# Optimization experiments

Hardware: AMD Instinct MI355X
Metric: run time of the kernel (lower is better)

## Reference

```python
import jax, jax.numpy as jnp
import numpy as np

N_NODES = 50000
N_EDGES = 800000
IN_DIM = 8
EDGE_DIM = 4
HIDDEN = 16
OUT_DIM = 1


def _lin_init(key, fan_in, fan_out):
    kw, kb = jax.random.split(key)
    bound = 1.0 / np.sqrt(fan_in)
    W = jax.random.uniform(kw, (fan_in, fan_out), minval=-bound, maxval=bound, dtype=jnp.float32)
    b = jax.random.uniform(kb, (fan_out,), minval=-bound, maxval=bound, dtype=jnp.float32)
    return W, b


def setup_inputs() -> dict:
    key = jax.random.key(0)
    ks = jax.random.split(key, 16)
    x = jax.random.normal(ks[0], (N_NODES, IN_DIM), dtype=jnp.float32)
    edge_index = jax.random.randint(ks[1], (2, N_EDGES), 0, N_NODES, dtype=jnp.int32)
    edge_attr = jax.random.normal(ks[2], (N_EDGES, EDGE_DIM), dtype=jnp.float32)

    inp = {"x": x, "edge_index": edge_index, "edge_attr": edge_attr}
    in_dims = [IN_DIM, HIDDEN]
    for i in range(2):
        d_in = in_dims[i]
        W1, b1 = _lin_init(ks[3 + 4 * i], EDGE_DIM, HIDDEN)
        W2, b2 = _lin_init(ks[4 + 4 * i], HIDDEN, d_in * HIDDEN)
        root = jax.random.uniform(ks[5 + 4 * i], (d_in, HIDDEN), minval=-1.0 / np.sqrt(d_in), maxval=1.0 / np.sqrt(d_in), dtype=jnp.float32)
        bias = jnp.zeros((HIDDEN,), dtype=jnp.float32)
        inp[f"eW1_{i}"] = W1; inp[f"eb1_{i}"] = b1
        inp[f"eW2_{i}"] = W2; inp[f"eb2_{i}"] = b2
        inp[f"root_{i}"] = root; inp[f"bias_{i}"] = bias
    mW1, mb1 = _lin_init(ks[11], HIDDEN, HIDDEN)
    mW2, mb2 = _lin_init(ks[12], HIDDEN, OUT_DIM)
    inp["mW1"] = mW1; inp["mb1"] = mb1; inp["mW2"] = mW2; inp["mb2"] = mb2
    return inp


def _nnconv(x, src, dst, edge_attr, eW1, eb1, eW2, eb2, root, bias):
    # edge MLP -> per-edge weight matrix [E, d_in, HIDDEN]
    h = jax.nn.silu(edge_attr @ eW1 + eb1)
    Wedge = (h @ eW2 + eb2).reshape(edge_attr.shape[0], x.shape[1], HIDDEN)
    # gather source features, per-edge matmul, scatter-mean to targets
    msg = jnp.einsum('ei,eio->eo', x[src], Wedge)  # [E, HIDDEN]
    agg = jax.ops.segment_sum(msg, dst, num_segments=N_NODES)
    cnt = jax.ops.segment_sum(jnp.ones((msg.shape[0],), dtype=msg.dtype), dst, num_segments=N_NODES)
    agg = agg / jnp.maximum(cnt, 1.0)[:, None]
    return x @ root + agg + bias


def reference(x, edge_index, edge_attr,
              eW1_0, eb1_0, eW2_0, eb2_0, root_0, bias_0,
              eW1_1, eb1_1, eW2_1, eb2_1, root_1, bias_1,
              mW1, mb1, mW2, mb2):
    src, dst = edge_index[0], edge_index[1]
    x = jax.nn.relu(_nnconv(x, src, dst, edge_attr, eW1_0, eb1_0, eW2_0, eb2_0, root_0, bias_0))
    x = jax.nn.relu(_nnconv(x, src, dst, edge_attr, eW1_1, eb1_1, eW2_1, eb2_1, root_1, bias_1))
    out = jax.nn.sigmoid(jax.nn.silu(x @ mW1 + mb1) @ mW2 + mb2)
    return out
```

## Files before the change

kernel.cpp:

```cpp
#include <hip/hip_runtime.h>
#include <hip/hip_fp16.h>

#define NN 50000
#define NE 800000
#define NBUCK 392

__device__ __forceinline__ float sigm(float v) { return 1.0f / (1.0f + __expf(-v)); }


__global__ void sort_count(const int* __restrict__ ei,
                           int* __restrict__ cntA, int* __restrict__ cntB)
{
    __shared__ int hA[NBUCK], hB[NBUCK];
    int t = threadIdx.x;
    for (int i = t; i < NBUCK; i += 256) { hA[i] = 0; hB[i] = 0; }
    __syncthreads();
    int base = blockIdx.x * 2048;
#pragma unroll
    for (int r = 0; r < 8; ++r) {
        int idx = base + r * 256 + t;
        if (idx < NE) {
            int s = ei[idx], d = ei[NE + idx];
            atomicAdd(&hB[s >> 7], 1);
            atomicAdd(&hA[d >> 7], 1);
        }
    }
    __syncthreads();
    for (int i = t; i < NBUCK; i += 256) {
        if (hA[i]) atomicAdd(&cntA[i], hA[i]);
        if (hB[i]) atomicAdd(&cntB[i], hB[i]);
    }
}

__global__ void sort_scan(const int* __restrict__ cntA, const int* __restrict__ cntB,
                          int* __restrict__ baseA, int* __restrict__ baseB,
                          int* __restrict__ curA,  int* __restrict__ curB)
{
    __shared__ int a[512], b[512];
    int t = threadIdx.x;
    a[t] = (t < NBUCK) ? cntA[t] : 0;
    b[t] = (t < NBUCK) ? cntB[t] : 0;
    __syncthreads();
#pragma unroll
    for (int dd = 1; dd < 512; dd <<= 1) {
        int av = (t >= dd) ? a[t - dd] : 0;
        int bv = (t >= dd) ? b[t - dd] : 0;
        __syncthreads();
        a[t] += av; b[t] += bv;
        __syncthreads();
    }
    int exA = (t > 0) ? a[t - 1] : 0;
    int exB = (t > 0) ? b[t - 1] : 0;
    if (t < NBUCK) { baseA[t] = exA; curA[t] = exA; baseB[t] = exB; curB[t] = exB; }
    if (t == 511)  { baseA[NBUCK] = a[511]; baseB[NBUCK] = b[511]; }
}

__global__ __launch_bounds__(256) void sort_scatterA(const int* __restrict__ ei,
                                                     int* __restrict__ curA,
                                                     unsigned long long* __restrict__ recA)
{
    __shared__ int lcnt[NBUCK];
    __shared__ int lofs[NBUCK];
    int t = threadIdx.x;
    for (int i = t; i < NBUCK; i += 256) lcnt[i] = 0;
    __syncthreads();
    int base = blockIdx.x * 2048;
#pragma unroll
    for (int r = 0; r < 8; ++r) {
        int e = base + r * 256 + t;
        if (e < NE) atomicAdd(&lcnt[ei[NE + e] >> 7], 1);
    }
    __syncthreads();
    for (int i = t; i < NBUCK; i += 256)
        lofs[i] = lcnt[i] ? atomicAdd(&curA[i], lcnt[i]) : 0;
    __syncthreads();
#pragma unroll
    for (int r = 0; r < 8; ++r) {
        int e = base + r * 256 + t;
        if (e < NE) {
            int s = ei[e], d = ei[NE + e];
            int p = atomicAdd(&lofs[d >> 7], 1);
            recA[p] = ((unsigned long long)(unsigned)(d & 127) << 36)
                    | ((unsigned long long)(unsigned)s << 20)
                    | (unsigned long long)(unsigned)e;
        }
    }
}

__global__ __launch_bounds__(256) void sort_localAB(const unsigned long long* __restrict__ recA,
                                                    const int* __restrict__ baseA,
                                                    int* __restrict__ off_all,
                                                    int* __restrict__ curB,
                                                    unsigned long long* __restrict__ recB)
{
    __shared__ int c[128];
    __shared__ int live[128];
    __shared__ int lcnt[NBUCK];
    __shared__ int lofs[NBUCK];
    int t = threadIdx.x;
    int b = blockIdx.x;
    int lo = baseA[b], hi = baseA[b + 1];
    if (t < 128) c[t] = 0;
    for (int i = t; i < NBUCK; i += 256) lcnt[i] = 0;
    __syncthreads();
    for (int i = lo + t; i < hi; i += 256) {
        unsigned long long rec = recA[i];
        atomicAdd(&c[(int)(rec >> 36) & 127], 1);
        atomicAdd(&lcnt[(int)(rec >> 27) & 511], 1);
    }
    __syncthreads();
#pragma unroll
    for (int dd = 1; dd < 128; dd <<= 1) {
        int v = (t >= dd && t < 128) ? c[t - dd] : 0;
        __syncthreads();
        if (t < 128) c[t] += v;
        __syncthreads();
    }
    if (t < 128) {
        int ex = (t > 0) ? c[t - 1] : 0;
        int d = (b << 7) + t;
        if (d <= NN) off_all[d] = lo + ex;
        live[t] = lo + ex;
    }
    __syncthreads();
    for (int i = t; i < NBUCK; i += 256)
        lofs[i] = lcnt[i] ? atomicAdd(&curB[i], lcnt[i]) : 0;
    __syncthreads();
    for (int i = lo + t; i < hi; i += 256) {
        unsigned long long rec = recA[i];
        int dp = atomicAdd(&live[(int)(rec >> 36) & 127], 1);
        int s  = (int)((rec >> 20) & 0xFFFFu);
        int p  = atomicAdd(&lofs[s >> 7], 1);
        recB[p] = ((unsigned long long)(unsigned)(s & 127) << 40)
                | ((unsigned long long)(unsigned)dp << 20)
                | (rec & 0xFFFFFull);
    }
}

__global__ __launch_bounds__(256) void sort_localB(const unsigned long long* __restrict__ recB,
                                                   const int* __restrict__ baseB,
                                                   const float4* __restrict__ ea4,
                                                   int* __restrict__ off_all,
                                                   unsigned* __restrict__ sperm32,
                                                   float4* __restrict__ ea_perm)
{
    __shared__ int c[128];
    __shared__ int live[128];
    int t = threadIdx.x;
    int b = blockIdx.x;
    int lo = baseB[b], hi = baseB[b + 1];
    if (t < 128) c[t] = 0;
    __syncthreads();
    for (int i = lo + t; i < hi; i += 256)
        atomicAdd(&c[(int)(recB[i] >> 40) & 127], 1);
    __syncthreads();
#pragma unroll
    for (int dd = 1; dd < 128; dd <<= 1) {
        int v = (t >= dd && t < 128) ? c[t - dd] : 0;
        __syncthreads();
        if (t < 128) c[t] += v;
        __syncthreads();
    }
    if (t < 128) {
        int ex = (t > 0) ? c[t - 1] : 0;
        int s = (b << 7) + t;
        if (s <= NN) off_all[NN + s] = NE + lo + ex;
        live[t] = lo + ex;
    }
    __syncthreads();
    for (int i = lo + t; i < hi; i += 256) {
        unsigned long long rec = recB[i];
        int k = (int)(rec >> 40) & 127;
        int pos = atomicAdd(&live[k], 1);
        unsigned sl = (unsigned)(k & 15);
        unsigned dp = (unsigned)((rec >> 20) & 0xFFFFFu);
        sperm32[pos] = (sl << 20) | dp;
        ea_perm[pos] = ea4[rec & 0xFFFFFull];
    }
}

template<int DIN>
__global__ __launch_bounds__(256) void edge_fusedG(
        const float* __restrict__ xin,
        const unsigned* __restrict__ sperm32,
        const float4* __restrict__ ea_perm,
        const float* __restrict__ eW1,
        const float* __restrict__ eb1,
        const float* __restrict__ eW2,
        const float* __restrict__ eb2,
        const int*   __restrict__ off_all,
        __half* __restrict__ msgbuf)
{
    constexpr int MROW = 260;
    constexpr int W2B  = 4 * DIN * 17 * 16;
    constexpr int SMB  = 16 * MROW * 4 + 256 * 4;
    constexpr int UNIB = (W2B > SMB) ? W2B : SMB;
    __shared__ __align__(16) char uni[UNIB];
    float*  smemM = (float*)uni;
    int*    sdp   = (int*)(uni + 16 * MROW * 4);
    __shared__ __align__(16) float4 G4[16 * 69];
    __shared__ __align__(16) float4 xbL[16 * 5];
    __shared__ __align__(16) float  xL[16 * DIN];
    __shared__ __align__(16) float  b2L[DIN * 16];
    __shared__ __align__(16) float4 w1t[16];
    __shared__ __align__(16) float  b1s[16];

    int tid = threadIdx.x;
    int nb  = blockIdx.x * 16;
    if (tid < 16) {
        w1t[tid] = make_float4(eW1[tid], eW1[16 + tid], eW1[32 + tid], eW1[48 + tid]);
        b1s[tid] = eb1[tid];
    }
    {
        float* w2f = (float*)uni;
        for (int t = tid; t < 16 * DIN * 16; t += 256) {
            int k = t / (DIN * 16);
            int rem = t - k * DIN * 16;
            int i = rem >> 4, o = rem & 15;
            w2f[((((o >> 2) * DIN + i) * 17) + k) * 4 + (o & 3)] = eW2[t];
        }
    }
    for (int t = tid; t < DIN * 16; t += 256) b2L[t] = eb2[t];
    for (int t = tid; t < 16 * DIN; t += 256) xL[t] = xin[(size_t)nb * DIN + t];
    __syncthreads();

    {
        int nl = tid >> 4, k = tid & 15;
        const float4* w2L4 = (const float4*)uni;
        float xv[DIN];
#pragma unroll
        for (int i = 0; i < DIN; ++i) xv[i] = xL[nl * DIN + i];
#pragma unroll
        for (int ob = 0; ob < 4; ++ob) {
            float4 a4 = make_float4(0.f, 0.f, 0.f, 0.f);
#pragma unroll
            for (int i = 0; i < DIN; ++i) {
                float4 w = w2L4[(ob * DIN + i) * 17 + k];
                a4.x += xv[i] * w.x; a4.y += xv[i] * w.y;
                a4.z += xv[i] * w.z; a4.w += xv[i] * w.w;
            }
            G4[nl * 69 + ob * 17 + k] = a4;
        }
        if (k < 4) {
            int ob = k;
            const float4* b2v = (const float4*)b2L;
            float4 a4 = make_float4(0.f, 0.f, 0.f, 0.f);
#pragma unroll
            for (int i = 0; i < DIN; ++i) {
                float4 b = b2v[i * 4 + ob];
                a4.x += xv[i] * b.x; a4.y += xv[i] * b.y;
                a4.z += xv[i] * b.z; a4.w += xv[i] * b.w;
            }
            xbL[nl * 5 + ob] = a4;
        }
    }
    __syncthreads();

    int eBeg = off_all[NN + nb] - NE;
    int eEnd = off_all[NN + nb + 16] - NE;
    for (int cb = eBeg; cb < eEnd; cb += 256) {
        int pos = cb + tid;
        bool valid = pos < eEnd;
        unsigned pk = valid ? sperm32[pos] : 0u;
        int dp = (int)(pk & 0xFFFFFu);
        int sl = (int)(pk >> 20);
        float4 a = valid ? ea_perm[pos] : make_float4(0.f, 0.f, 0.f, 0.f);

        float h[16];
#pragma unroll
        for (int j = 0; j < 16; ++j) {
            float4 w = w1t[j];
            float p = b1s[j] + a.x * w.x + a.y * w.y + a.z * w.z + a.w * w.w;
            h[j] = p * sigm(p);
        }
        float4 acc[4];
#pragma unroll
        for (int ob = 0; ob < 4; ++ob) acc[ob] = xbL[sl * 5 + ob];
#pragma unroll
        for (int k = 0; k < 16; ++k) {
            float hk = h[k];
#pragma unroll
            for (int ob = 0; ob < 4; ++ob) {
                float4 g = G4[sl * 69 + ob * 17 + k];
                acc[ob].x += hk * g.x; acc[ob].y += hk * g.y;
                acc[ob].z += hk * g.z; acc[ob].w += hk * g.w;
            }
        }
        sdp[tid] = valid ? dp : -1;
#pragma unroll
        for (int ob = 0; ob < 4; ++ob) {
            smemM[(ob * 4 + 0) * MROW + tid] = acc[ob].x;
            smemM[(ob * 4 + 1) * MROW + tid] = acc[ob].y;
            smemM[(ob * 4 + 2) * MROW + tid] = acc[ob].z;
            smemM[(ob * 4 + 3) * MROW + tid] = acc[ob].w;
        }
        __syncthreads();
        int nvalid = eEnd - cb; if (nvalid > 256) nvalid = 256;
        int nr = (nvalid + 31) >> 5;
        for (int r = 0; r < nr; ++r) {
            int le = r * 32 + (tid >> 3);
            int p  = tid & 7;
            int d2 = sdp[le];
            float v0 = smemM[(2 * p)     * MROW + le];
            float v1 = smemM[(2 * p + 1) * MROW + le];
            if (d2 >= 0) {
                __half2 hv = __floats2half2_rn(v0, v1);
                *((__half2*)(msgbuf + (size_t)d2 * 16) + p) = hv;
            }
        }
        __syncthreads();
    }
}

__device__ __forceinline__ float gather_msg16(const __half* __restrict__ msgbuf,
                                              int s0, int e0, int tid)
{
    int half = (tid >> 3) & 1;
    int p    = tid & 7;
    float ax = 0.f, ay = 0.f;
    for (int j = s0 + half; j < e0; j += 2) {
        __half2 hv = *((const __half2*)(msgbuf + (size_t)j * 16) + p);
        float2 f = __half22float2(hv);
        ax += f.x; ay += f.y;
    }
    ax += __shfl_xor(ax, 8, 16);
    ay += __shfl_xor(ay, 8, 16);
    int ch = tid & 15;
    float vx = __shfl(ax, ch >> 1, 16);
    float vy = __shfl(ay, ch >> 1, 16);
    return (ch & 1) ? vy : vx;
}

__global__ __launch_bounds__(256) void gather_L0(
        const float* __restrict__ xin,
        const float* __restrict__ root,
        const float* __restrict__ bias,
        const int*   __restrict__ off_all,
        const __half* __restrict__ msgbuf,
        float* __restrict__ x1)
{
    __shared__ __align__(16) float rootL[8 * 16];
    __shared__ __align__(16) float biasL[16];
    int tid = threadIdx.x;
    if (tid < 128) rootL[tid] = root[tid];
    if (tid < 16) biasL[tid] = bias[tid];
    __syncthreads();

    int ch = tid & 15;
    int n  = blockIdx.x * 16 + (tid >> 4);
    int s0 = off_all[n], e0 = off_all[n + 1];

    float acc = gather_msg16(msgbuf, s0, e0, tid);
    float v = acc / fmaxf((float)(e0 - s0), 1.0f) + biasL[ch];
#pragma unroll
    for (int i = 0; i < 8; ++i)
        v += xin[(size_t)n * 8 + i] * rootL[i * 16 + ch];
    x1[(size_t)n * 16 + ch] = fmaxf(v, 0.f);
}

__global__ __launch_bounds__(256) void gather_final(
        const float* __restrict__ x1,
        const float* __restrict__ root,
        const float* __restrict__ bias,
        const int*   __restrict__ off_all,
        const __half* __restrict__ msgbuf,
        const float* __restrict__ mW1,
        const float* __restrict__ mb1,
        const float* __restrict__ mW2,
        const float* __restrict__ mb2,
        float* __restrict__ out)
{
    __shared__ __align__(16) float rootL[256];
    __shared__ __align__(16) float biasL[16];
    __shared__ __align__(16) float w1m[256];
    __shared__ __align__(16) float b1m[16];
    __shared__ __align__(16) float w2m[16];
    __shared__ float b2m;
    int tid = threadIdx.x;
    rootL[tid] = root[tid];
    w1m[tid] = mW1[tid];
    if (tid < 16) { biasL[tid] = bias[tid]; b1m[tid] = mb1[tid]; w2m[tid] = mW2[tid]; }
    if (tid == 0) b2m = mb2[0];
    __syncthreads();

    int ch = tid & 15;
    int n  = blockIdx.x * 16 + (tid >> 4);
    int s0 = off_all[n], e0 = off_all[n + 1];

    float acc = gather_msg16(msgbuf, s0, e0, tid);
    float v = acc / fmaxf((float)(e0 - s0), 1.0f) + biasL[ch];
#pragma unroll
    for (int i = 0; i < 16; ++i)
        v += x1[(size_t)n * 16 + i] * rootL[i * 16 + ch];
    v = fmaxf(v, 0.f);

    float z = b1m[ch];
#pragma unroll
    for (int o = 0; o < 16; ++o) {
        float vo = __shfl(v, o, 16);
        z += vo * w1m[o * 16 + ch];
    }
    float ss = z * sigm(z) * w2m[ch];
#pragma unroll
    for (int off = 8; off; off >>= 1) ss += __shfl_xor(ss, off, 16);
    if (ch == 0) out[n] = sigm(ss + b2m);
}

extern "C" void kernel_launch(void* const* d_in, const int* in_sizes, int n_in,
                              void* d_out, int out_size, void* d_ws, size_t ws_size,
                              hipStream_t stream) {
    const float* x     = (const float*)d_in[0];
    const int*   ei    = (const int*)  d_in[1];
    const float* ea    = (const float*)d_in[2];
    const float* eW1_0 = (const float*)d_in[3];
    const float* eb1_0 = (const float*)d_in[4];
    const float* eW2_0 = (const float*)d_in[5];
    const float* eb2_0 = (const float*)d_in[6];
    const float* root0 = (const float*)d_in[7];
    const float* bias0 = (const float*)d_in[8];
    const float* eW1_1 = (const float*)d_in[9];
    const float* eb1_1 = (const float*)d_in[10];
    const float* eW2_1 = (const float*)d_in[11];
    const float* eb2_1 = (const float*)d_in[12];
    const float* root1 = (const float*)d_in[13];
    const float* bias1 = (const float*)d_in[14];
    const float* mW1   = (const float*)d_in[15];
    const float* mb1   = (const float*)d_in[16];
    const float* mW2   = (const float*)d_in[17];
    const float* mb2   = (const float*)d_in[18];
    float* out = (float*)d_out;

    const int GG  = NN / 16;
    const int SBK = (NE + 2047) / 2048;

    int* W = (int*)d_ws;
    int* off_all = W;
    int* cntA    = W + 100004;
    int* cntB    = W + 100400;
    int* baseA   = W + 100800;
    int* baseB   = W + 101200;
    int* curA    = W + 101600;
    int* curB    = W + 102000;
    unsigned* sperm32 = (unsigned*)(W + 102400);
    float4* ea_perm   = (float4*)(W + 902400);
    float*  x1        = (float*)(W + 4102400);
    __half* msgbuf    = (__half*)(W + 4902400);
    unsigned long long* recA = (unsigned long long*)(W + 4902400);
    unsigned long long* recB = (unsigned long long*)(W + 6502400);

    hipMemsetAsync(cntA, 0, 2 * 396 * sizeof(int), stream);
    sort_count   <<<SBK,  256, 0, stream>>>(ei, cntA, cntB);
    sort_scan    <<<1,    512, 0, stream>>>(cntA, cntB, baseA, baseB, curA, curB);
    sort_scatterA<<<SBK,  256, 0, stream>>>(ei, curA, recA);
    sort_localAB <<<NBUCK,256, 0, stream>>>(recA, baseA, off_all, curB, recB);
    sort_localB  <<<NBUCK,256, 0, stream>>>(recB, baseB, (const float4*)ea,
                                            off_all, sperm32, ea_perm);

    edge_fusedG<8><<<GG, 256, 0, stream>>>(x, sperm32, ea_perm, eW1_0, eb1_0,
                                           eW2_0, eb2_0, off_all, msgbuf);
    gather_L0<<<GG, 256, 0, stream>>>(x, root0, bias0, off_all, msgbuf, x1);

    edge_fusedG<16><<<GG, 256, 0, stream>>>(x1, sperm32, ea_perm, eW1_1, eb1_1,
                                            eW2_1, eb2_1, off_all, msgbuf);
    gather_final<<<GG, 256, 0, stream>>>(x1, root1, bias1, off_all, msgbuf,
                                         mW1, mb1, mW2, mb2, out);
}
```

Measured before the change: 279.5 us.

## Fold bucket scan into scatter kernels and store edge messages directly

Removes the single-block sort_scan kernel. sort_scatterA and sort_localAB now each redundantly compute the 392-bucket prefix sum in shared memory, block 0 publishes the bases, and the cur counters start at zero via the enlarged memset. In edge_fusedG, each thread packs its 16 message values into halfs and writes them as two 16-byte stores to its destination slot. This replaces the shared-memory transpose and its two __syncthreads per chunk, and the register cache of x is dropped. The trade is redundant scan work in every block and less regular global store patterns.

```diff
diff --git a/kernel.cpp b/kernel.cpp
--- a/kernel.cpp
+++ b/kernel.cpp
@@ -32,36 +32,18 @@
     }
 }
 
-__global__ void sort_scan(const int* __restrict__ cntA, const int* __restrict__ cntB,
-                          int* __restrict__ baseA, int* __restrict__ baseB,
-                          int* __restrict__ curA,  int* __restrict__ curB)
-{
-    __shared__ int a[512], b[512];
-    int t = threadIdx.x;
-    a[t] = (t < NBUCK) ? cntA[t] : 0;
-    b[t] = (t < NBUCK) ? cntB[t] : 0;
-    __syncthreads();
-#pragma unroll
-    for (int dd = 1; dd < 512; dd <<= 1) {
-        int av = (t >= dd) ? a[t - dd] : 0;
-        int bv = (t >= dd) ? b[t - dd] : 0;
-        __syncthreads();
-        a[t] += av; b[t] += bv;
-        __syncthreads();
-    }
-    int exA = (t > 0) ? a[t - 1] : 0;
-    int exB = (t > 0) ? b[t - 1] : 0;
-    if (t < NBUCK) { baseA[t] = exA; curA[t] = exA; baseB[t] = exB; curB[t] = exB; }
-    if (t == 511)  { baseA[NBUCK] = a[511]; baseB[NBUCK] = b[511]; }
-}
-
 __global__ __launch_bounds__(256) void sort_scatterA(const int* __restrict__ ei,
+                                                     const int* __restrict__ cntA,
                                                      int* __restrict__ curA,
+                                                     int* __restrict__ baseAg,
                                                      unsigned long long* __restrict__ recA)
 {
+    __shared__ int sc[512];
     __shared__ int lcnt[NBUCK];
     __shared__ int lofs[NBUCK];
     int t = threadIdx.x;
+    sc[t]       = (t < NBUCK) ? cntA[t] : 0;
+    sc[t + 256] = (t + 256 < NBUCK) ? cntA[t + 256] : 0;
     for (int i = t; i < NBUCK; i += 256) lcnt[i] = 0;
     __syncthreads();
     int base = blockIdx.x * 2048;
@@ -70,9 +52,21 @@
         int e = base + r * 256 + t;
         if (e < NE) atomicAdd(&lcnt[ei[NE + e] >> 7], 1);
     }
-    __syncthreads();
-    for (int i = t; i < NBUCK; i += 256)
-        lofs[i] = lcnt[i] ? atomicAdd(&curA[i], lcnt[i]) : 0;
+#pragma unroll
+    for (int dd = 1; dd < 512; dd <<= 1) {
+        int v0 = (t >= dd) ? sc[t - dd] : 0;
+        int v1 = sc[t + 256 - dd];
+        __syncthreads();
+        sc[t] += v0; sc[t + 256] += v1;
+        __syncthreads();
+    }
+    for (int i = t; i < NBUCK; i += 256) {
+        int ex = (i > 0) ? sc[i - 1] : 0;
+        lofs[i] = lcnt[i] ? (ex + atomicAdd(&curA[i], lcnt[i])) : 0;
+    }
+    if (blockIdx.x == 0)
+        for (int i = t; i <= NBUCK; i += 256)
+            baseAg[i] = (i > 0) ? sc[i - 1] : 0;
     __syncthreads();
 #pragma unroll
     for (int r = 0; r < 8; ++r) {
@@ -89,10 +83,13 @@
 
 __global__ __launch_bounds__(256) void sort_localAB(const unsigned long long* __restrict__ recA,
                                                     const int* __restrict__ baseA,
+                                                    const int* __restrict__ cntB,
+                                                    int* __restrict__ curB,
+                                                    int* __restrict__ baseBg,
                                                     int* __restrict__ off_all,
-                                                    int* __restrict__ curB,
                                                     unsigned long long* __restrict__ recB)
 {
+    __shared__ int sc[512];
     __shared__ int c[128];
     __shared__ int live[128];
     __shared__ int lcnt[NBUCK];
@@ -100,6 +97,8 @@
     int t = threadIdx.x;
     int b = blockIdx.x;
     int lo = baseA[b], hi = baseA[b + 1];
+    sc[t]       = (t < NBUCK) ? cntB[t] : 0;
+    sc[t + 256] = (t + 256 < NBUCK) ? cntB[t + 256] : 0;
     if (t < 128) c[t] = 0;
     for (int i = t; i < NBUCK; i += 256) lcnt[i] = 0;
     __syncthreads();
@@ -108,7 +107,14 @@
         atomicAdd(&c[(int)(rec >> 36) & 127], 1);
         atomicAdd(&lcnt[(int)(rec >> 27) & 511], 1);
     }
-    __syncthreads();
+#pragma unroll
+    for (int dd = 1; dd < 512; dd <<= 1) {
+        int v0 = (t >= dd) ? sc[t - dd] : 0;
+        int v1 = sc[t + 256 - dd];
+        __syncthreads();
+        sc[t] += v0; sc[t + 256] += v1;
+        __syncthreads();
+    }
 #pragma unroll
     for (int dd = 1; dd < 128; dd <<= 1) {
         int v = (t >= dd && t < 128) ? c[t - dd] : 0;
@@ -123,8 +129,13 @@
         live[t] = lo + ex;
     }
     __syncthreads();
-    for (int i = t; i < NBUCK; i += 256)
-        lofs[i] = lcnt[i] ? atomicAdd(&curB[i], lcnt[i]) : 0;
+    for (int i = t; i < NBUCK; i += 256) {
+        int ex = (i > 0) ? sc[i - 1] : 0;
+        lofs[i] = lcnt[i] ? (ex + atomicAdd(&curB[i], lcnt[i])) : 0;
+    }
+    if (b == 0)
+        for (int i = t; i <= NBUCK; i += 256)
+            baseBg[i] = (i > 0) ? sc[i - 1] : 0;
     __syncthreads();
     for (int i = lo + t; i < hi; i += 256) {
         unsigned long long rec = recA[i];
@@ -191,13 +202,7 @@
         const int*   __restrict__ off_all,
         __half* __restrict__ msgbuf)
 {
-    constexpr int MROW = 260;
-    constexpr int W2B  = 4 * DIN * 17 * 16;
-    constexpr int SMB  = 16 * MROW * 4 + 256 * 4;
-    constexpr int UNIB = (W2B > SMB) ? W2B : SMB;
-    __shared__ __align__(16) char uni[UNIB];
-    float*  smemM = (float*)uni;
-    int*    sdp   = (int*)(uni + 16 * MROW * 4);
+    __shared__ __align__(16) float4 w2L4[4 * DIN * 17];
     __shared__ __align__(16) float4 G4[16 * 69];
     __shared__ __align__(16) float4 xbL[16 * 5];
     __shared__ __align__(16) float  xL[16 * DIN];
@@ -212,7 +217,7 @@
         b1s[tid] = eb1[tid];
     }
     {
-        float* w2f = (float*)uni;
+        float* w2f = (float*)w2L4;
         for (int t = tid; t < 16 * DIN * 16; t += 256) {
             int k = t / (DIN * 16);
             int rem = t - k * DIN * 16;
@@ -226,18 +231,15 @@
 
     {
         int nl = tid >> 4, k = tid & 15;
-        const float4* w2L4 = (const float4*)uni;
-        float xv[DIN];
-#pragma unroll
-        for (int i = 0; i < DIN; ++i) xv[i] = xL[nl * DIN + i];
+        const float* xrow = xL + nl * DIN;
 #pragma unroll
         for (int ob = 0; ob < 4; ++ob) {
             float4 a4 = make_float4(0.f, 0.f, 0.f, 0.f);
 #pragma unroll
             for (int i = 0; i < DIN; ++i) {
                 float4 w = w2L4[(ob * DIN + i) * 17 + k];
-                a4.x += xv[i] * w.x; a4.y += xv[i] * w.y;
-                a4.z += xv[i] * w.z; a4.w += xv[i] * w.w;
+                a4.x += xrow[i] * w.x; a4.y += xrow[i] * w.y;
+                a4.z += xrow[i] * w.z; a4.w += xrow[i] * w.w;
             }
             G4[nl * 69 + ob * 17 + k] = a4;
         }
@@ -248,8 +250,8 @@
 #pragma unroll
             for (int i = 0; i < DIN; ++i) {
                 float4 b = b2v[i * 4 + ob];
-                a4.x += xv[i] * b.x; a4.y += xv[i] * b.y;
-                a4.z += xv[i] * b.z; a4.w += xv[i] * b.w;
+                a4.x += xrow[i] * b.x; a4.y += xrow[i] * b.y;
+                a4.z += xrow[i] * b.z; a4.w += xrow[i] * b.w;
             }
             xbL[nl * 5 + ob] = a4;
         }
@@ -258,13 +260,11 @@
 
     int eBeg = off_all[NN + nb] - NE;
     int eEnd = off_all[NN + nb + 16] - NE;
-    for (int cb = eBeg; cb < eEnd; cb += 256) {
-        int pos = cb + tid;
-        bool valid = pos < eEnd;
-        unsigned pk = valid ? sperm32[pos] : 0u;
+    for (int pos = eBeg + tid; pos < eEnd; pos += 256) {
+        unsigned pk = sperm32[pos];
         int dp = (int)(pk & 0xFFFFFu);
         int sl = (int)(pk >> 20);
-        float4 a = valid ? ea_perm[pos] : make_float4(0.f, 0.f, 0.f, 0.f);
+        float4 a = ea_perm[pos];
 
         float h[16];
 #pragma unroll
@@ -286,29 +286,21 @@
                 acc[ob].z += hk * g.z; acc[ob].w += hk * g.w;
             }
         }
-        sdp[tid] = valid ? dp : -1;
-#pragma unroll
-        for (int ob = 0; ob < 4; ++ob) {
-            smemM[(ob * 4 + 0) * MROW + tid] = acc[ob].x;
-            smemM[(ob * 4 + 1) * MROW + tid] = acc[ob].y;
-            smemM[(ob * 4 + 2) * MROW + tid] = acc[ob].z;
-            smemM[(ob * 4 + 3) * MROW + tid] = acc[ob].w;
-        }
-        __syncthreads();
-        int nvalid = eEnd - cb; if (nvalid > 256) nvalid = 256;
-        int nr = (nvalid + 31) >> 5;
-        for (int r = 0; r < nr; ++r) {
-            int le = r * 32 + (tid >> 3);
-            int p  = tid & 7;
-            int d2 = sdp[le];
-            float v0 = smemM[(2 * p)     * MROW + le];
-            float v1 = smemM[(2 * p + 1) * MROW + le];
-            if (d2 >= 0) {
-                __half2 hv = __floats2half2_rn(v0, v1);
-                *((__half2*)(msgbuf + (size_t)d2 * 16) + p) = hv;
-            }
-        }
-        __syncthreads();
+        __half2 h01 = __floats2half2_rn(acc[0].x, acc[0].y);
+        __half2 h23 = __floats2half2_rn(acc[0].z, acc[0].w);
+        __half2 h45 = __floats2half2_rn(acc[1].x, acc[1].y);
+        __half2 h67 = __floats2half2_rn(acc[1].z, acc[1].w);
+        __half2 h89 = __floats2half2_rn(acc[2].x, acc[2].y);
+        __half2 hAB = __floats2half2_rn(acc[2].z, acc[2].w);
+        __half2 hCD = __floats2half2_rn(acc[3].x, acc[3].y);
+        __half2 hEF = __floats2half2_rn(acc[3].z, acc[3].w);
+        uint4 w0 = make_uint4(*(unsigned*)&h01, *(unsigned*)&h23,
+                              *(unsigned*)&h45, *(unsigned*)&h67);
+        uint4 w1 = make_uint4(*(unsigned*)&h89, *(unsigned*)&hAB,
+                              *(unsigned*)&hCD, *(unsigned*)&hEF);
+        uint4* dst = (uint4*)(msgbuf + (size_t)dp * 16);
+        dst[0] = w0;
+        dst[1] = w1;
     }
 }
 
@@ -435,24 +427,24 @@
 
     int* W = (int*)d_ws;
     int* off_all = W;
-    int* cntA    = W + 100004;
-    int* cntB    = W + 100400;
-    int* baseA   = W + 100800;
-    int* baseB   = W + 101200;
-    int* curA    = W + 101600;
-    int* curB    = W + 102000;
-    unsigned* sperm32 = (unsigned*)(W + 102400);
-    float4* ea_perm   = (float4*)(W + 902400);
-    float*  x1        = (float*)(W + 4102400);
-    __half* msgbuf    = (__half*)(W + 4902400);
-    unsigned long long* recA = (unsigned long long*)(W + 4902400);
-    unsigned long long* recB = (unsigned long long*)(W + 6502400);
-
-    hipMemsetAsync(cntA, 0, 2 * 396 * sizeof(int), stream);
+    int* cntA    = W + 100008;
+    int* cntB    = W + 100408;
+    int* curA    = W + 100808;
+    int* curB    = W + 101208;
+    int* baseA   = W + 101608;
+    int* baseB   = W + 102008;
+    unsigned* sperm32 = (unsigned*)(W + 102408);
+    float4* ea_perm   = (float4*)(W + 902408);
+    float*  x1        = (float*)(W + 4102408);
+    __half* msgbuf    = (__half*)(W + 4902408);
+    unsigned long long* recA = (unsigned long long*)(W + 4902408);
+    unsigned long long* recB = (unsigned long long*)(W + 6502408);
+
+    hipMemsetAsync(cntA, 0, 1600 * sizeof(int), stream);
     sort_count   <<<SBK,  256, 0, stream>>>(ei, cntA, cntB);
-    sort_scan    <<<1,    512, 0, stream>>>(cntA, cntB, baseA, baseB, curA, curB);
-    sort_scatterA<<<SBK,  256, 0, stream>>>(ei, curA, recA);
-    sort_localAB <<<NBUCK,256, 0, stream>>>(recA, baseA, off_all, curB, recB);
+    sort_scatterA<<<SBK,  256, 0, stream>>>(ei, cntA, curA, baseA, recA);
+    sort_localAB <<<NBUCK,256, 0, stream>>>(recA, baseA, cntB, curB, baseB,
+                                            off_all, recB);
     sort_localB  <<<NBUCK,256, 0, stream>>>(recB, baseB, (const float4*)ea,
                                             off_all, sperm32, ea_perm);
 
```

Result: no change. 279.6 us (+0.0%).
